# Kernel optimization log

Hardware: AMD Instinct MI355X
Metric: run time of the kernel (lower is better)

Reference implementation:

```python
import jax, jax.numpy as jnp
import numpy as np

B = 256          # batch of images
TOK = 256        # 16x16 tokens per image
V = 1024         # codebook size
D = 256          # code dim


def setup_inputs() -> dict:
    key = jax.random.key(0)
    k1, k2, k3, k4 = jax.random.split(key, 4)
    image_seq = jax.random.randint(k1, (B, TOK), 0, V, dtype=jnp.int64)
    image_seq2 = jax.random.randint(k2, (B, TOK), 0, V, dtype=jnp.int64)
    alpha = jax.random.uniform(k3, (1,), dtype=jnp.float32)
    W = jax.random.normal(k4, (V, D), dtype=jnp.float32)
    return {"image_seq": image_seq, "image_seq2": image_seq2, "alpha": alpha, "W": W}


def reference(image_seq, image_seq2, alpha, W):
    a = alpha[0]
    # gather codebook entries: [B, TOK, D]
    emb = W[image_seq]
    emb2 = W[image_seq2]
    x = (1.0 - a) * emb + a * emb2
    xf = x.reshape(-1, D)                        # [N, D], N = B*TOK
    # brute-force L2 distance to every code, without materializing [N, V, D]:
    d = (jnp.sum(xf * xf, axis=-1, keepdims=True)
         - 2.0 * xf @ W.T
         + jnp.sum(W * W, axis=-1)[None, :])
    idx = jnp.argmin(d, axis=1)                  # top-1 nearest code, [N]
    # get_codebook_entry: gather, reshape to bhwc, permute to bchw
    z_q = W[idx].reshape(B, 16, 16, D)           # [B, 16, 16, 256]
    z_q = jnp.transpose(z_q, (0, 3, 1, 2))       # [B, 256, 16, 16]
    return z_q
```

## Files before the change

kernel.cpp:

```cpp
#include <hip/hip_runtime.h>

static constexpr int Vn = 1024;
static constexpr int Dn = 256;
static constexpr int NT = 65536;

typedef float vfloat4 __attribute__((ext_vector_type(4)));

__global__ __launch_bounds__(256) void gram_kernel(const float* __restrict__ W,
                                                   float* __restrict__ G,
                                                   float* __restrict__ norms) {
    __shared__ float As[32][68];
    __shared__ float Bs[32][68];
    const int tid = threadIdx.x;
    const int tx = tid & 15;
    const int ty = tid >> 4;
    const int bm = blockIdx.y * 64;
    const int bn = blockIdx.x * 64;
    const float4* Wv = (const float4*)W;

    const int m0  = tid >> 3;
    const int kql = tid & 7;

    float4 pa[2], pb[2];
#pragma unroll
    for (int s = 0; s < 2; ++s) {
        pa[s] = Wv[(bm + m0 + 32 * s) * 64 + kql];
        pb[s] = Wv[(bn + m0 + 32 * s) * 64 + kql];
    }

    float acc[4][4] = {};
    for (int c = 0; c < 8; ++c) {
#pragma unroll
        for (int s = 0; s < 2; ++s) {
            const int m = m0 + 32 * s;
            As[kql * 4 + 0][m] = pa[s].x;
            As[kql * 4 + 1][m] = pa[s].y;
            As[kql * 4 + 2][m] = pa[s].z;
            As[kql * 4 + 3][m] = pa[s].w;
            Bs[kql * 4 + 0][m] = pb[s].x;
            Bs[kql * 4 + 1][m] = pb[s].y;
            Bs[kql * 4 + 2][m] = pb[s].z;
            Bs[kql * 4 + 3][m] = pb[s].w;
        }
        __syncthreads();
        if (c < 7) {
            const int kq = (c + 1) * 8 + kql;
#pragma unroll
            for (int s = 0; s < 2; ++s) {
                pa[s] = Wv[(bm + m0 + 32 * s) * 64 + kq];
                pb[s] = Wv[(bn + m0 + 32 * s) * 64 + kq];
            }
        }
        const float* Ab = &As[0][ty * 4];
        const float* Bb = &Bs[0][tx * 4];
        float4 a_c = *(const float4*)Ab;
        float4 b_c = *(const float4*)Bb;
#pragma unroll
        for (int kk = 0; kk < 32; ++kk) {
            const int kn = (kk < 31) ? kk + 1 : kk;
            const float4 a_n = *(const float4*)(Ab + kn * 68);
            const float4 b_n = *(const float4*)(Bb + kn * 68);
            const float a_s[4] = {a_c.x, a_c.y, a_c.z, a_c.w};
            const float b_s[4] = {b_c.x, b_c.y, b_c.z, b_c.w};
#pragma unroll
            for (int u = 0; u < 4; ++u)
#pragma unroll
                for (int w = 0; w < 4; ++w)
                    acc[u][w] = fmaf(a_s[u], b_s[w], acc[u][w]);
            a_c = a_n;
            b_c = b_n;
        }
        __syncthreads();
    }
#pragma unroll
    for (int u = 0; u < 4; ++u) {
        const int row = bm + ty * 4 + u;
        vfloat4 o;
        o.x = acc[u][0]; o.y = acc[u][1]; o.z = acc[u][2]; o.w = acc[u][3];
        __builtin_nontemporal_store(o, (vfloat4*)(G + row * Vn + bn + tx * 4));
        if (bm == bn && tx == ty) norms[row] = acc[u][u];
    }
}

__global__ __launch_bounds__(256) void argmin_write_kernel(const int* __restrict__ seq,
                                                           const int* __restrict__ seq2,
                                                           const float* __restrict__ alpha,
                                                           const float* __restrict__ G,
                                                           const float* __restrict__ norms,
                                                           const float* __restrict__ W,
                                                           float* __restrict__ out) {
    __shared__ float T[32][129];
    __shared__ int bestVs[32];
    const int tid = threadIdx.x;
    const int wave = tid >> 6;
    const int lane = tid & 63;
    const int t0 = blockIdx.x * 32;

    float4 nn_r[4];
#pragma unroll
    for (int s = 0; s < 4; ++s) nn_r[s] = ((const float4*)norms)[s * 64 + lane];

    const float a = alpha[0];
    const float c0 = -2.0f * (1.0f - a);
    const float c1 = -2.0f * a;

    for (int bb = 0; bb < 2; ++bb) {
        const int base_t = t0 + wave * 8 + bb * 4;
        const int base_l = wave * 8 + bb * 4;
        int iv[4], jv[4];
#pragma unroll
        for (int q = 0; q < 4; ++q) { iv[q] = seq[base_t + q]; jv[q] = seq2[base_t + q]; }
#pragma unroll
        for (int pair = 0; pair < 2; ++pair) {
            const int qa = pair * 2, qb = pair * 2 + 1;
            const float4* GiA = (const float4*)(G + iv[qa] * Vn);
            const float4* GjA = (const float4*)(G + jv[qa] * Vn);
            const float4* GiB = (const float4*)(G + iv[qb] * Vn);
            const float4* GjB = (const float4*)(G + jv[qb] * Vn);
            float4 gia[4], gja[4], gib[4], gjb[4];
#pragma unroll
            for (int s = 0; s < 4; ++s) {
                const int e = s * 64 + lane;
                gia[s] = GiA[e];
                gja[s] = GjA[e];
                gib[s] = GiB[e];
                gjb[s] = GjB[e];
            }
            float bestA = __builtin_inff(), bestB = __builtin_inff();
            int vA = 0, vB = 0;
#pragma unroll
            for (int s = 0; s < 4; ++s) {
                const int e = s * 64 + lane;
                const float4 nn = nn_r[s];
                const int v = e * 4;
                {
                    const float s0 = fmaf(c1, gja[s].x, fmaf(c0, gia[s].x, nn.x));
                    const float s1 = fmaf(c1, gja[s].y, fmaf(c0, gia[s].y, nn.y));
                    const float s2 = fmaf(c1, gja[s].z, fmaf(c0, gia[s].z, nn.z));
                    const float s3 = fmaf(c1, gja[s].w, fmaf(c0, gia[s].w, nn.w));
                    if (s0 < bestA) { bestA = s0; vA = v; }
                    if (s1 < bestA) { bestA = s1; vA = v + 1; }
                    if (s2 < bestA) { bestA = s2; vA = v + 2; }
                    if (s3 < bestA) { bestA = s3; vA = v + 3; }
                }
                {
                    const float s0 = fmaf(c1, gjb[s].x, fmaf(c0, gib[s].x, nn.x));
                    const float s1 = fmaf(c1, gjb[s].y, fmaf(c0, gib[s].y, nn.y));
                    const float s2 = fmaf(c1, gjb[s].z, fmaf(c0, gib[s].z, nn.z));
                    const float s3 = fmaf(c1, gjb[s].w, fmaf(c0, gib[s].w, nn.w));
                    if (s0 < bestB) { bestB = s0; vB = v; }
                    if (s1 < bestB) { bestB = s1; vB = v + 1; }
                    if (s2 < bestB) { bestB = s2; vB = v + 2; }
                    if (s3 < bestB) { bestB = s3; vB = v + 3; }
                }
            }
#pragma unroll
            for (int off = 32; off >= 1; off >>= 1) {
                const float oa = __shfl_down(bestA, off, 64);
                const int   va = __shfl_down(vA, off, 64);
                if (oa < bestA || (oa == bestA && va < vA)) { bestA = oa; vA = va; }
                const float ob = __shfl_down(bestB, off, 64);
                const int   vb = __shfl_down(vB, off, 64);
                if (ob < bestB || (ob == bestB && vb < vB)) { bestB = ob; vB = vb; }
            }
            if (lane == 0) {
                bestVs[base_l + qa] = vA;
                bestVs[base_l + qb] = vB;
            }
        }
    }
    __syncthreads();

    const int b   = t0 >> 8;
    const int hw0 = t0 & 255;
    float* outb = out + b * 65536 + hw0;
    const int tok = tid >> 3;
    const int l8  = tid & 7;
    const int hw4  = (tid & 7) * 4;
    const int drow = tid >> 3;
#pragma unroll
    for (int half = 0; half < 2; ++half) {
        const int v = bestVs[tok];
        const float4* Wr = (const float4*)(W + v * Dn + half * 128);
#pragma unroll
        for (int p = 0; p < 4; ++p) {
            const int d4 = p * 8 + l8;
            const float4 w4 = Wr[d4];
            T[tok][d4 * 4 + 0] = w4.x;
            T[tok][d4 * 4 + 1] = w4.y;
            T[tok][d4 * 4 + 2] = w4.z;
            T[tok][d4 * 4 + 3] = w4.w;
        }
        __syncthreads();
#pragma unroll
        for (int dp = 0; dp < 128; dp += 32) {
            const int dl = dp + drow;
            const int d = half * 128 + dl;
            vfloat4 o;
            o.x = T[hw4 + 0][dl];
            o.y = T[hw4 + 1][dl];
            o.z = T[hw4 + 2][dl];
            o.w = T[hw4 + 3][dl];
            __builtin_nontemporal_store(o, (vfloat4*)(outb + d * 256 + hw4));
        }
        __syncthreads();
    }
}

extern "C" void kernel_launch(void* const* d_in, const int* in_sizes, int n_in,
                              void* d_out, int out_size, void* d_ws, size_t ws_size,
                              hipStream_t stream) {
    const int*   seq   = (const int*)d_in[0];
    const int*   seq2  = (const int*)d_in[1];
    const float* alpha = (const float*)d_in[2];
    const float* W     = (const float*)d_in[3];
    float* out = (float*)d_out;

    char* ws = (char*)d_ws;
    float* G     = (float*)(ws);
    float* norms = (float*)(ws + 4194304);

    gram_kernel<<<dim3(16, 16), 256, 0, stream>>>(W, G, norms);
    argmin_write_kernel<<<NT / 32, 256, 0, stream>>>(seq, seq2, alpha, G, norms, W, out);
}
```

Baseline: 124.3 us.

## Bucket tokens by first code index to reuse Gram rows in registers

Splits the argmin+write kernel into a per-code bucket kernel and a separate write kernel. Each block owns one code c, holds G[c] in registers, scans the whole seq array with ballots to find matching tokens, and computes their argmin loading only the G row of seq2. This aims to halve Gram-row reads, at the cost of every block scanning all token indices, serial per-token processing within a wave, and an extra launch with an index round trip through global memory.

Measured after the change: 158.4 us. +27.4%, slower.

```diff
diff --git a/kernel.cpp b/kernel.cpp
--- a/kernel.cpp
+++ b/kernel.cpp
@@ -82,105 +82,92 @@
     }
 }
 
-__global__ __launch_bounds__(256) void argmin_write_kernel(const int* __restrict__ seq,
-                                                           const int* __restrict__ seq2,
-                                                           const float* __restrict__ alpha,
-                                                           const float* __restrict__ G,
-                                                           const float* __restrict__ norms,
-                                                           const float* __restrict__ W,
-                                                           float* __restrict__ out) {
-    __shared__ float T[32][129];
-    __shared__ int bestVs[32];
-    const int tid = threadIdx.x;
-    const int wave = tid >> 6;
+__global__ __launch_bounds__(256) void argmin_bucket_kernel(const int* __restrict__ seq,
+                                                            const int* __restrict__ seq2,
+                                                            const float* __restrict__ alpha,
+                                                            const float* __restrict__ G,
+                                                            const float* __restrict__ norms,
+                                                            int* __restrict__ bestV) {
+    const int c    = blockIdx.x;
+    const int tid  = threadIdx.x;
+    const int w    = tid >> 6;
     const int lane = tid & 63;
-    const int t0 = blockIdx.x * 32;
-
-    float4 nn_r[4];
-#pragma unroll
-    for (int s = 0; s < 4; ++s) nn_r[s] = ((const float4*)norms)[s * 64 + lane];
-
-    const float a = alpha[0];
+
+    float4 nn_r[4], gi_r[4];
+    const float4* Gi = (const float4*)(G + c * Vn);
+#pragma unroll
+    for (int s = 0; s < 4; ++s) {
+        nn_r[s] = ((const float4*)norms)[s * 64 + lane];
+        gi_r[s] = Gi[s * 64 + lane];
+    }
+
+    const float a  = alpha[0];
     const float c0 = -2.0f * (1.0f - a);
     const float c1 = -2.0f * a;
 
-    for (int bb = 0; bb < 2; ++bb) {
-        const int base_t = t0 + wave * 8 + bb * 4;
-        const int base_l = wave * 8 + bb * 4;
-        int iv[4], jv[4];
-#pragma unroll
-        for (int q = 0; q < 4; ++q) { iv[q] = seq[base_t + q]; jv[q] = seq2[base_t + q]; }
-#pragma unroll
-        for (int pair = 0; pair < 2; ++pair) {
-            const int qa = pair * 2, qb = pair * 2 + 1;
-            const float4* GiA = (const float4*)(G + iv[qa] * Vn);
-            const float4* GjA = (const float4*)(G + jv[qa] * Vn);
-            const float4* GiB = (const float4*)(G + iv[qb] * Vn);
-            const float4* GjB = (const float4*)(G + jv[qb] * Vn);
-            float4 gia[4], gja[4], gib[4], gjb[4];
-#pragma unroll
-            for (int s = 0; s < 4; ++s) {
-                const int e = s * 64 + lane;
-                gia[s] = GiA[e];
-                gja[s] = GjA[e];
-                gib[s] = GiB[e];
-                gjb[s] = GjB[e];
+    const int4* seq4 = (const int4*)seq;
+    for (int it = 0; it < 64; ++it) {
+        const int idx4 = tid + 256 * it;
+        const int4 v4 = seq4[idx4];
+        const int sub = (v4.x == c ? 1 : 0) | (v4.y == c ? 2 : 0) |
+                        (v4.z == c ? 4 : 0) | (v4.w == c ? 8 : 0);
+        unsigned long long mask = __ballot(sub != 0);
+        while (mask) {
+            const int src = __builtin_ctzll((unsigned long long)mask);
+            mask &= mask - 1;
+            const int smask = __shfl(sub, src, 64);
+            const int tbase = 4 * (w * 64 + src + 256 * it);
+#pragma unroll
+            for (int q = 0; q < 4; ++q) {
+                if (!(smask & (1 << q))) continue;
+                const int t = tbase + q;
+                const int j = seq2[t];
+                const float4* Gj = (const float4*)(G + j * Vn);
+                float best = __builtin_inff();
+                int vbest = 0;
+#pragma unroll
+                for (int s = 0; s < 4; ++s) {
+                    const float4 gj = Gj[s * 64 + lane];
+                    const float4 gi = gi_r[s];
+                    const float4 nn = nn_r[s];
+                    const int v = (s * 64 + lane) * 4;
+                    const float s0 = fmaf(c1, gj.x, fmaf(c0, gi.x, nn.x));
+                    const float s1 = fmaf(c1, gj.y, fmaf(c0, gi.y, nn.y));
+                    const float s2 = fmaf(c1, gj.z, fmaf(c0, gi.z, nn.z));
+                    const float s3 = fmaf(c1, gj.w, fmaf(c0, gi.w, nn.w));
+                    if (s0 < best) { best = s0; vbest = v; }
+                    if (s1 < best) { best = s1; vbest = v + 1; }
+                    if (s2 < best) { best = s2; vbest = v + 2; }
+                    if (s3 < best) { best = s3; vbest = v + 3; }
+                }
+#pragma unroll
+                for (int off = 32; off >= 1; off >>= 1) {
+                    const float ob = __shfl_down(best, off, 64);
+                    const int   vb = __shfl_down(vbest, off, 64);
+                    if (ob < best || (ob == best && vb < vbest)) { best = ob; vbest = vb; }
+                }
+                if (lane == 0) bestV[t] = vbest;
             }
-            float bestA = __builtin_inff(), bestB = __builtin_inff();
-            int vA = 0, vB = 0;
-#pragma unroll
-            for (int s = 0; s < 4; ++s) {
-                const int e = s * 64 + lane;
-                const float4 nn = nn_r[s];
-                const int v = e * 4;
-                {
-                    const float s0 = fmaf(c1, gja[s].x, fmaf(c0, gia[s].x, nn.x));
-                    const float s1 = fmaf(c1, gja[s].y, fmaf(c0, gia[s].y, nn.y));
-                    const float s2 = fmaf(c1, gja[s].z, fmaf(c0, gia[s].z, nn.z));
-                    const float s3 = fmaf(c1, gja[s].w, fmaf(c0, gia[s].w, nn.w));
-                    if (s0 < bestA) { bestA = s0; vA = v; }
-                    if (s1 < bestA) { bestA = s1; vA = v + 1; }
-                    if (s2 < bestA) { bestA = s2; vA = v + 2; }
-                    if (s3 < bestA) { bestA = s3; vA = v + 3; }
-                }
-                {
-                    const float s0 = fmaf(c1, gjb[s].x, fmaf(c0, gib[s].x, nn.x));
-                    const float s1 = fmaf(c1, gjb[s].y, fmaf(c0, gib[s].y, nn.y));
-                    const float s2 = fmaf(c1, gjb[s].z, fmaf(c0, gib[s].z, nn.z));
-                    const float s3 = fmaf(c1, gjb[s].w, fmaf(c0, gib[s].w, nn.w));
-                    if (s0 < bestB) { bestB = s0; vB = v; }
-                    if (s1 < bestB) { bestB = s1; vB = v + 1; }
-                    if (s2 < bestB) { bestB = s2; vB = v + 2; }
-                    if (s3 < bestB) { bestB = s3; vB = v + 3; }
-                }
-            }
-#pragma unroll
-            for (int off = 32; off >= 1; off >>= 1) {
-                const float oa = __shfl_down(bestA, off, 64);
-                const int   va = __shfl_down(vA, off, 64);
-                if (oa < bestA || (oa == bestA && va < vA)) { bestA = oa; vA = va; }
-                const float ob = __shfl_down(bestB, off, 64);
-                const int   vb = __shfl_down(vB, off, 64);
-                if (ob < bestB || (ob == bestB && vb < vB)) { bestB = ob; vB = vb; }
-            }
-            if (lane == 0) {
-                bestVs[base_l + qa] = vA;
-                bestVs[base_l + qb] = vB;
-            }
-        }
-    }
-    __syncthreads();
-
+        }
+    }
+}
+
+__global__ __launch_bounds__(256) void write_kernel(const int* __restrict__ bestV,
+                                                    const float* __restrict__ W,
+                                                    float* __restrict__ out) {
+    __shared__ float T[32][129];
+    const int tid = threadIdx.x;
+    const int t0  = blockIdx.x * 32;
     const int b   = t0 >> 8;
     const int hw0 = t0 & 255;
     float* outb = out + b * 65536 + hw0;
-    const int tok = tid >> 3;
-    const int l8  = tid & 7;
+    const int tok  = tid >> 3;
+    const int l8   = tid & 7;
     const int hw4  = (tid & 7) * 4;
     const int drow = tid >> 3;
+    const int v = bestV[t0 + tok];
 #pragma unroll
     for (int half = 0; half < 2; ++half) {
-        const int v = bestVs[tok];
         const float4* Wr = (const float4*)(W + v * Dn + half * 128);
 #pragma unroll
         for (int p = 0; p < 4; ++p) {
@@ -219,7 +206,9 @@
     char* ws = (char*)d_ws;
     float* G     = (float*)(ws);
     float* norms = (float*)(ws + 4194304);
+    int*   bestV = (int*)(ws + 4194304 + 4096);
 
     gram_kernel<<<dim3(16, 16), 256, 0, stream>>>(W, G, norms);
-    argmin_write_kernel<<<NT / 32, 256, 0, stream>>>(seq, seq2, alpha, G, norms, W, out);
-}
+    argmin_bucket_kernel<<<Vn, 256, 0, stream>>>(seq, seq2, alpha, G, norms, bestV);
+    write_kernel<<<NT / 32, 256, 0, stream>>>(bestV, W, out);
+}
```
